# Optimization experiments

Measured on AMD Instinct MI355X. Metric: run time of the kernel, lower is better.

The kernel has to match this reference:

```python
import jax, jax.numpy as jnp
import numpy as np

H = 256       # hidden_dim
E = H // 2    # operator embedding dim
T = 12        # num_tempers
O = 3         # num_ops per temper
HOPS = 4      # max_path_hops
B = 128       # batch
D = 2048      # input_dim
NCLS = 10     # task_head classes


def setup_inputs() -> dict:
    key = jax.random.key(0)
    ks = jax.random.split(key, 12)
    x = jax.random.normal(ks[0], (B, D), jnp.float32)
    N = B * (D // H)  # 1024 patch tokens
    # per-hop routed temper per patch; value == T means halt
    sampled_tempers = jax.random.randint(ks[1], (HOPS, N), 0, T + 1, jnp.int32)
    sampled_ops = jax.random.randint(ks[2], (HOPS, N), 0, O, jnp.int32)
    s1 = 1.0 / np.sqrt(H + E)
    W1 = jax.random.uniform(ks[3], (T, O, H + E, H), jnp.float32, -s1, s1)
    b1 = jax.random.uniform(ks[4], (T, O, H), jnp.float32, -s1, s1)
    s2 = 1.0 / np.sqrt(H)
    W2 = jax.random.uniform(ks[5], (T, O, H, H), jnp.float32, -s2, s2)
    b2 = jax.random.uniform(ks[6], (T, O, H), jnp.float32, -s2, s2)
    op_emb = jax.random.normal(ks[7], (T, O, E), jnp.float32)
    ln_g = jnp.ones((H,), jnp.float32)
    ln_b = jnp.zeros((H,), jnp.float32)
    Wt = jax.random.uniform(ks[8], (H, NCLS), jnp.float32, -s2, s2)
    bt = jax.random.uniform(ks[9], (NCLS,), jnp.float32, -s2, s2)
    return dict(x=x, W1=W1, b1=b1, W2=W2, b2=b2, op_emb=op_emb,
                ln_g=ln_g, ln_b=ln_b, Wt=Wt, bt=bt,
                sampled_tempers=sampled_tempers, sampled_ops=sampled_ops)


def reference(x, W1, b1, W2, b2, op_emb, ln_g, ln_b, Wt, bt,
              sampled_tempers, sampled_ops):
    Bsz, Din = x.shape
    pad = (-Din) % H
    if pad > 0:
        x = jnp.pad(x, ((0, 0), (0, pad)))
    state = x.reshape(-1, H)                       # [N, H] patch states
    active = jnp.ones((state.shape[0],), bool)     # not-yet-halted mask
    for hop in range(HOPS):
        t = sampled_tempers[hop]
        o = sampled_ops[hop]
        active = active & (t != T)                 # T == halt action
        tc = jnp.clip(t, 0, T - 1)                 # safe index for halted rows
        emb = op_emb[tc, o]                        # [N, E] op embedding gather
        xa = jnp.concatenate([state, emb], axis=-1)  # [N, H+E]
        # per-token expert weight gather + batched matvec (memory-bound dispatch)
        h = jax.nn.relu(jnp.einsum('ni,nio->no', xa, W1[tc, o]) + b1[tc, o])
        y = jax.nn.relu(jnp.einsum('ni,nio->no', h, W2[tc, o]) + b2[tc, o])
        state = jnp.where(active[:, None], y, state)
    pooled = state.reshape(Bsz, -1, H).mean(axis=1)   # [B, H]
    mu = pooled.mean(axis=-1, keepdims=True)
    var = pooled.var(axis=-1, keepdims=True)
    normed = (pooled - mu) * jax.lax.rsqrt(var + 1e-5) * ln_g + ln_b
    return normed @ Wt + bt                           # [B, 10]
```

## Files before the change

kernel.cpp:

```cpp
#include <hip/hip_runtime.h>

typedef __attribute__((ext_vector_type(8))) short short8;
typedef __attribute__((ext_vector_type(4))) float floatx4;

#define NEXP   36
#define NTOK   1024
#define HOPS   4

#define OFF_STATE   0u
#define OFF_W1B     1048576u
#define OFF_W2B     5767168u
#define OFF_C1      10485760u
#define OFF_COUNTS  10522624u
#define OFF_LISTS   10523264u

__device__ __forceinline__ unsigned short f2bf(float f) {
    unsigned u = __float_as_uint(f);
    u += 0x7FFFu + ((u >> 16) & 1u);
    return (unsigned short)(u >> 16);
}

__global__ __launch_bounds__(256) void prep_kernel(
    const float* __restrict__ W1, const float* __restrict__ b1,
    const float* __restrict__ W2, const float* __restrict__ op_emb,
    const int* __restrict__ tempers, const int* __restrict__ ops,
    unsigned short* __restrict__ W1b, unsigned short* __restrict__ W2b,
    float* __restrict__ c1, int* __restrict__ counts, int* __restrict__ lists)
{
    const int bid = blockIdx.x;
    const int t = threadIdx.x;

    if (bid < 2880) {
        const int r  = bid & 7;
        const int q  = bid >> 3;
        const int e  = r + 8 * (q >> 6);
        if (e >= NEXP) return;
        const int sub = q & 63;
        const int mat = sub >> 5;
        const int s2  = sub & 31;
        const int kb  = s2 >> 2;
        const int jt  = s2 & 3;
        const float* src = mat ? (W2 + e * 65536) : (W1 + e * 98304);
        unsigned short* dst = (mat ? W2b : W1b) + e * 65536;
        const int j  = jt * 64 + (t & 63);
        const int ks = (t >> 6) * 8;
        short8 v;
        #pragma unroll
        for (int i = 0; i < 8; i++)
            v[i] = (short)f2bf(src[(kb * 32 + ks + i) * 256 + j]);
        *(short8*)(dst + (kb * 256 + j) * 32 + ks) = v;
    } else if (bid < 2916) {
        const int e = bid - 2880;
        __shared__ float eb[128];
        if (t < 128) eb[t] = op_emb[e * 128 + t];
        __syncthreads();
        float acc = b1[e * 256 + t];
        const float* wp = W1 + e * 98304 + 65536;
        #pragma unroll 4
        for (int k = 0; k < 128; k++)
            acc += eb[k] * wp[k * 256 + t];
        c1[e * 256 + t] = acc;
    } else {
        __shared__ int lc[HOPS * NEXP];
        if (t < HOPS * NEXP) lc[t] = 0;
        __syncthreads();
        for (int q = 0; q < 4; q++) {
            int n = q * 256 + t;
            bool act = true;
            for (int hop = 0; hop < HOPS; hop++) {
                int tt = tempers[hop * NTOK + n];
                int oo = ops[hop * NTOK + n];
                act = act && (tt != 12);
                if (act) {
                    int e = tt * 3 + oo;
                    int pos = atomicAdd(&lc[hop * NEXP + e], 1);
                    lists[(hop * NEXP + e) * NTOK + pos] = n;
                }
            }
        }
        __syncthreads();
        if (t < HOPS * NEXP) counts[t] = lc[t];
    }
}

__global__ __launch_bounds__(1024, 4) void hop_kernel(
    const float* __restrict__ src, float* __restrict__ state,
    const unsigned short* __restrict__ W1b,
    const unsigned short* __restrict__ W2b,
    const float* __restrict__ c1, const float* __restrict__ b2,
    const int* __restrict__ counts, const int* __restrict__ lists, int hop)
{
    const int e    = blockIdx.x % 40;
    const int slot = blockIdx.x / 40;
    if (e >= NEXP) return;
    const int n_e = counts[hop * NEXP + e];
    if (slot * 16 >= n_e) return;

    const int t = threadIdx.x;
    const int l = t & 63, w = t >> 6;
    const int col = l & 15, g = l >> 4;
    const int j = w * 16 + col;

    const unsigned short* Wp  = W1b + e * 65536;
    const unsigned short* Wp2 = W2b + e * 65536;
    short8 B1[8], B2[8];
    #pragma unroll
    for (int kb = 0; kb < 8; kb++) {
        B1[kb] = *(const short8*)(Wp  + (kb * 256 + j) * 32 + g * 8);
        B2[kb] = *(const short8*)(Wp2 + (kb * 256 + j) * 32 + g * 8);
    }
    #pragma unroll
    for (int kb = 0; kb < 8; kb++) {
        asm volatile("" : "+v"(B1[kb]));
        asm volatile("" : "+v"(B2[kb]));
    }
    const float cv = c1[e * 256 + j];
    const float bv = b2[e * 256 + j];

    __shared__ int toks[16];
    __shared__ unsigned short Ab[4096];
    __shared__ unsigned short Hb[4096];

    for (int m0 = slot * 16; m0 < n_e; m0 += 64) {
        const int mact = min(16, n_e - m0);
        __syncthreads();
        if (t < 16)
            toks[t] = (t < mact) ? lists[(hop * NEXP + e) * NTOK + m0 + t] : 0;
        __syncthreads();

        {
            int m = t >> 6;
            int k = (t & 63) * 4;
            float4 v = make_float4(0.f, 0.f, 0.f, 0.f);
            if (m < mact) v = *(const float4*)(src + toks[m] * 256 + k);
            int kb = k >> 5, gg = (k >> 3) & 3, i = k & 7;
            unsigned short* d = Ab + kb * 512 + (gg * 16 + m) * 8 + i;
            d[0] = f2bf(v.x); d[1] = f2bf(v.y); d[2] = f2bf(v.z); d[3] = f2bf(v.w);
        }
        __syncthreads();

        floatx4 acc = (floatx4){cv, cv, cv, cv};
        #pragma unroll
        for (int kb = 0; kb < 8; kb++) {
            short8 a = *(const short8*)(Ab + kb * 512 + l * 8);
            acc = __builtin_amdgcn_mfma_f32_16x16x32_bf16(a, B1[kb], acc, 0, 0, 0);
        }
        {
            int kb2 = j >> 5, g2 = (j >> 3) & 3, i2 = j & 7;
            #pragma unroll
            for (int r = 0; r < 4; r++) {
                int m = g * 4 + r;
                float vv = acc[r];
                vv = vv > 0.f ? vv : 0.f;
                Hb[kb2 * 512 + (g2 * 16 + m) * 8 + i2] = f2bf(vv);
            }
        }
        __syncthreads();

        floatx4 acc2 = (floatx4){bv, bv, bv, bv};
        #pragma unroll
        for (int kb = 0; kb < 8; kb++) {
            short8 a = *(const short8*)(Hb + kb * 512 + l * 8);
            acc2 = __builtin_amdgcn_mfma_f32_16x16x32_bf16(a, B2[kb], acc2, 0, 0, 0);
        }
        #pragma unroll
        for (int r = 0; r < 4; r++) {
            int m = g * 4 + r;
            if (m < mact) {
                float vv = acc2[r];
                state[toks[m] * 256 + j] = vv > 0.f ? vv : 0.f;
            }
        }
    }
}

__global__ __launch_bounds__(256) void final_kernel(
    const float* __restrict__ x, const float* __restrict__ state,
    const int* __restrict__ tempers,
    const float* __restrict__ ln_g, const float* __restrict__ ln_b,
    const float* __restrict__ Wt, const float* __restrict__ bt,
    float* __restrict__ out)
{
    const int b = blockIdx.x, t = threadIdx.x;
    float s = 0.f;
    #pragma unroll
    for (int p = 0; p < 8; p++) {
        int n = b * 8 + p;
        const float* rowsrc = (tempers[n] != 12) ? state : x;
        s += rowsrc[n * 256 + t];
    }
    s *= 0.125f;

    float v1 = s, v2 = s * s;
    #pragma unroll
    for (int off = 32; off; off >>= 1) {
        v1 += __shfl_down(v1, off);
        v2 += __shfl_down(v2, off);
    }
    __shared__ float red[8];
    __shared__ float stats[2];
    const int w = t >> 6, l = t & 63;
    if (l == 0) { red[w] = v1; red[4 + w] = v2; }
    __syncthreads();
    if (t == 0) {
        float su = red[0] + red[1] + red[2] + red[3];
        float sq = red[4] + red[5] + red[6] + red[7];
        float mu = su * (1.0f / 256.0f);
        float var = sq * (1.0f / 256.0f) - mu * mu;
        stats[0] = mu;
        stats[1] = rsqrtf(var + 1e-5f);
    }
    __syncthreads();
    float normed = (s - stats[0]) * stats[1] * ln_g[t] + ln_b[t];

    __shared__ float pr[40];
    #pragma unroll
    for (int c = 0; c < 10; c++) {
        float pv = normed * Wt[t * 10 + c];
        #pragma unroll
        for (int off = 32; off; off >>= 1) pv += __shfl_down(pv, off);
        if (l == 0) pr[w * 10 + c] = pv;
    }
    __syncthreads();
    if (t < 10)
        out[b * 10 + t] = pr[t] + pr[10 + t] + pr[20 + t] + pr[30 + t] + bt[t];
}

extern "C" void kernel_launch(void* const* d_in, const int* in_sizes, int n_in,
                              void* d_out, int out_size, void* d_ws, size_t ws_size,
                              hipStream_t stream)
{
    const float* x      = (const float*)d_in[0];
    const float* W1     = (const float*)d_in[1];
    const float* b1     = (const float*)d_in[2];
    const float* W2     = (const float*)d_in[3];
    const float* b2     = (const float*)d_in[4];
    const float* op_emb = (const float*)d_in[5];
    const float* ln_g   = (const float*)d_in[6];
    const float* ln_b   = (const float*)d_in[7];
    const float* Wt     = (const float*)d_in[8];
    const float* bt     = (const float*)d_in[9];
    const int* tempers  = (const int*)d_in[10];
    const int* ops      = (const int*)d_in[11];

    char* ws = (char*)d_ws;
    float* state          = (float*)(ws + OFF_STATE);
    unsigned short* W1b   = (unsigned short*)(ws + OFF_W1B);
    unsigned short* W2b   = (unsigned short*)(ws + OFF_W2B);
    float* c1             = (float*)(ws + OFF_C1);
    int* counts           = (int*)(ws + OFF_COUNTS);
    int* lists            = (int*)(ws + OFF_LISTS);
    float* out            = (float*)d_out;

    prep_kernel<<<2917, 256, 0, stream>>>(W1, b1, W2, op_emb, tempers, ops,
                                          W1b, W2b, c1, counts, lists);
    for (int hop = 0; hop < HOPS; hop++)
        hop_kernel<<<160, 1024, 0, stream>>>(hop == 0 ? x : state, state,
                                             W1b, W2b, c1, b2,
                                             counts, lists, hop);
    final_kernel<<<128, 256, 0, stream>>>(x, state, tempers,
                                          ln_g, ln_b, Wt, bt, out);
}
```

Before: 138.1 us.

## Fuse four hop launches into one persistent kernel with per-token version flags

Replaces the four per-hop kernel launches with a single kernel that loops over hops. Ordering between hops is kept by a per-token version counter: each 16-token chunk spin-waits until its tokens were written in the previous hop, then bumps their counters after writing. This removes three launch gaps and lets each block load its expert weights into registers once instead of four times. In exchange it adds spin-wait and fence overhead, and it relies on all 160 blocks being co-resident to avoid deadlock.

```diff
diff --git a/kernel.cpp b/kernel.cpp
--- a/kernel.cpp
+++ b/kernel.cpp
@@ -13,6 +13,7 @@
 #define OFF_C1      10485760u
 #define OFF_COUNTS  10522624u
 #define OFF_LISTS   10523264u
+#define OFF_VER     11113088u
 
 __device__ __forceinline__ unsigned short f2bf(float f) {
     unsigned u = __float_as_uint(f);
@@ -25,7 +26,8 @@
     const float* __restrict__ W2, const float* __restrict__ op_emb,
     const int* __restrict__ tempers, const int* __restrict__ ops,
     unsigned short* __restrict__ W1b, unsigned short* __restrict__ W2b,
-    float* __restrict__ c1, int* __restrict__ counts, int* __restrict__ lists)
+    float* __restrict__ c1, int* __restrict__ counts, int* __restrict__ lists,
+    int* __restrict__ ver)
 {
     const int bid = blockIdx.x;
     const int t = threadIdx.x;
@@ -63,6 +65,7 @@
     } else {
         __shared__ int lc[HOPS * NEXP];
         if (t < HOPS * NEXP) lc[t] = 0;
+        for (int i = t; i < NTOK; i += 256) ver[i] = 0;
         __syncthreads();
         for (int q = 0; q < 4; q++) {
             int n = q * 256 + t;
@@ -83,18 +86,26 @@
     }
 }
 
-__global__ __launch_bounds__(1024, 4) void hop_kernel(
-    const float* __restrict__ src, float* __restrict__ state,
+__global__ __launch_bounds__(1024, 4) void mega_hop_kernel(
+    const float* __restrict__ x, float* __restrict__ state,
     const unsigned short* __restrict__ W1b,
     const unsigned short* __restrict__ W2b,
     const float* __restrict__ c1, const float* __restrict__ b2,
-    const int* __restrict__ counts, const int* __restrict__ lists, int hop)
+    const int* __restrict__ counts, const int* __restrict__ lists,
+    int* __restrict__ ver)
 {
     const int e    = blockIdx.x % 40;
     const int slot = blockIdx.x / 40;
     if (e >= NEXP) return;
-    const int n_e = counts[hop * NEXP + e];
-    if (slot * 16 >= n_e) return;
+
+    int ne[HOPS];
+    bool any = false;
+    #pragma unroll
+    for (int h = 0; h < HOPS; h++) {
+        ne[h] = counts[h * NEXP + e];
+        any = any || (slot * 16 < ne[h]);
+    }
+    if (!any) return;
 
     const int t = threadIdx.x;
     const int l = t & 63, w = t >> 6;
@@ -121,54 +132,77 @@
     __shared__ unsigned short Ab[4096];
     __shared__ unsigned short Hb[4096];
 
-    for (int m0 = slot * 16; m0 < n_e; m0 += 64) {
-        const int mact = min(16, n_e - m0);
-        __syncthreads();
-        if (t < 16)
-            toks[t] = (t < mact) ? lists[(hop * NEXP + e) * NTOK + m0 + t] : 0;
-        __syncthreads();
-
-        {
-            int m = t >> 6;
-            int k = (t & 63) * 4;
-            float4 v = make_float4(0.f, 0.f, 0.f, 0.f);
-            if (m < mact) v = *(const float4*)(src + toks[m] * 256 + k);
-            int kb = k >> 5, gg = (k >> 3) & 3, i = k & 7;
-            unsigned short* d = Ab + kb * 512 + (gg * 16 + m) * 8 + i;
-            d[0] = f2bf(v.x); d[1] = f2bf(v.y); d[2] = f2bf(v.z); d[3] = f2bf(v.w);
-        }
-        __syncthreads();
-
-        floatx4 acc = (floatx4){cv, cv, cv, cv};
-        #pragma unroll
-        for (int kb = 0; kb < 8; kb++) {
-            short8 a = *(const short8*)(Ab + kb * 512 + l * 8);
-            acc = __builtin_amdgcn_mfma_f32_16x16x32_bf16(a, B1[kb], acc, 0, 0, 0);
-        }
-        {
-            int kb2 = j >> 5, g2 = (j >> 3) & 3, i2 = j & 7;
+    for (int hop = 0; hop < HOPS; hop++) {
+        const float* src = hop ? state : x;
+        for (int m0 = slot * 16; m0 < ne[hop]; m0 += 64) {
+            const int mact = min(16, ne[hop] - m0);
+            __syncthreads();
+            if (t < 16) {
+                int tok = (t < mact)
+                        ? lists[(hop * NEXP + e) * NTOK + m0 + t] : -1;
+                toks[t] = tok;
+                if (hop > 0 && tok >= 0) {
+                    while (__hip_atomic_load(&ver[tok], __ATOMIC_RELAXED,
+                                             __HIP_MEMORY_SCOPE_AGENT) < hop)
+                        __builtin_amdgcn_s_sleep(1);
+                    (void)__hip_atomic_load(&ver[tok], __ATOMIC_ACQUIRE,
+                                            __HIP_MEMORY_SCOPE_AGENT);
+                }
+            }
+            __syncthreads();
+
+            {
+                int m = t >> 6;
+                int k = (t & 63) * 4;
+                float4 v = make_float4(0.f, 0.f, 0.f, 0.f);
+                if (m < mact) v = *(const float4*)(src + toks[m] * 256 + k);
+                int kb = k >> 5, gg = (k >> 3) & 3, i = k & 7;
+                unsigned short* d = Ab + kb * 512 + (gg * 16 + m) * 8 + i;
+                d[0] = f2bf(v.x); d[1] = f2bf(v.y);
+                d[2] = f2bf(v.z); d[3] = f2bf(v.w);
+            }
+            __syncthreads();
+
+            floatx4 acc = (floatx4){cv, cv, cv, cv};
+            #pragma unroll
+            for (int kb = 0; kb < 8; kb++) {
+                short8 a = *(const short8*)(Ab + kb * 512 + l * 8);
+                acc = __builtin_amdgcn_mfma_f32_16x16x32_bf16(a, B1[kb], acc, 0, 0, 0);
+            }
+            {
+                int kb2 = j >> 5, g2 = (j >> 3) & 3, i2 = j & 7;
+                #pragma unroll
+                for (int r = 0; r < 4; r++) {
+                    int m = g * 4 + r;
+                    float vv = acc[r];
+                    vv = vv > 0.f ? vv : 0.f;
+                    Hb[kb2 * 512 + (g2 * 16 + m) * 8 + i2] = f2bf(vv);
+                }
+            }
+            __syncthreads();
+
+            floatx4 acc2 = (floatx4){bv, bv, bv, bv};
+            #pragma unroll
+            for (int kb = 0; kb < 8; kb++) {
+                short8 a = *(const short8*)(Hb + kb * 512 + l * 8);
+                acc2 = __builtin_amdgcn_mfma_f32_16x16x32_bf16(a, B2[kb], acc2, 0, 0, 0);
+            }
             #pragma unroll
             for (int r = 0; r < 4; r++) {
                 int m = g * 4 + r;
-                float vv = acc[r];
-                vv = vv > 0.f ? vv : 0.f;
-                Hb[kb2 * 512 + (g2 * 16 + m) * 8 + i2] = f2bf(vv);
-            }
-        }
-        __syncthreads();
-
-        floatx4 acc2 = (floatx4){bv, bv, bv, bv};
-        #pragma unroll
-        for (int kb = 0; kb < 8; kb++) {
-            short8 a = *(const short8*)(Hb + kb * 512 + l * 8);
-            acc2 = __builtin_amdgcn_mfma_f32_16x16x32_bf16(a, B2[kb], acc2, 0, 0, 0);
-        }
-        #pragma unroll
-        for (int r = 0; r < 4; r++) {
-            int m = g * 4 + r;
-            if (m < mact) {
-                float vv = acc2[r];
-                state[toks[m] * 256 + j] = vv > 0.f ? vv : 0.f;
+                if (m < mact) {
+                    float vv = acc2[r];
+                    state[toks[m] * 256 + j] = vv > 0.f ? vv : 0.f;
+                }
+            }
+
+            if (hop < HOPS - 1) {
+                __syncthreads();
+                if (t == 0) __threadfence();
+                __syncthreads();
+                if (t < mact)
+                    __hip_atomic_fetch_add(&ver[toks[t]], 1, __ATOMIC_RELEASE,
+                                           __HIP_MEMORY_SCOPE_AGENT);
             }
         }
     }
@@ -250,14 +284,13 @@
     float* c1             = (float*)(ws + OFF_C1);
     int* counts           = (int*)(ws + OFF_COUNTS);
     int* lists            = (int*)(ws + OFF_LISTS);
+    int* ver              = (int*)(ws + OFF_VER);
     float* out            = (float*)d_out;
 
     prep_kernel<<<2917, 256, 0, stream>>>(W1, b1, W2, op_emb, tempers, ops,
-                                          W1b, W2b, c1, counts, lists);
-    for (int hop = 0; hop < HOPS; hop++)
-        hop_kernel<<<160, 1024, 0, stream>>>(hop == 0 ? x : state, state,
-                                             W1b, W2b, c1, b2,
-                                             counts, lists, hop);
+                                          W1b, W2b, c1, counts, lists, ver);
+    mega_hop_kernel<<<160, 1024, 0, stream>>>(x, state, W1b, W2b, c1, b2,
+                                              counts, lists, ver);
     final_kernel<<<128, 256, 0, stream>>>(x, state, tempers,
                                           ln_g, ln_b, Wt, bt, out);
 }
```

Result: faster. 135.4 us (-2.0%).
